# Optimization experiments

Measured on AMD Instinct MI355X. Metric: run time of the kernel, lower is better.

## Reference

```python
import jax, jax.numpy as jnp
import numpy as np

NUM_USERS = 100000
NUM_ITEMS = 50000
N = NUM_USERS + NUM_ITEMS
EMB = 64
NNZ = 4000000
B = 4096
GAMMA = 1.0
REG_LAMBDA = 1e-4
T_END = 1.0  # Euler step size: t = [0, 1]
EPS = 1e-12


def setup_inputs() -> dict:
    key = jax.random.key(0)
    ks = jax.random.split(key, 8)
    user = jax.random.randint(ks[0], (B,), 0, NUM_USERS)
    positive = jax.random.randint(ks[1], (B,), 0, NUM_ITEMS)
    negative = jax.random.randint(ks[2], (B,), 0, NUM_ITEMS)
    adj_rows = jax.random.randint(ks[3], (NNZ,), 0, N)
    adj_cols = jax.random.randint(ks[4], (NNZ,), 0, N)
    # normalized-adjacency-like small positive values
    adj_vals = jax.random.uniform(ks[5], (NNZ,), jnp.float32) * 1e-3
    user_emb = jax.random.normal(ks[6], (NUM_USERS, EMB), jnp.float32) * 0.1
    item_emb = jax.random.normal(ks[7], (NUM_ITEMS, EMB), jnp.float32) * 0.1
    return {
        "user": user, "positive": positive, "negative": negative,
        "adj_rows": adj_rows, "adj_cols": adj_cols, "adj_vals": adj_vals,
        "user_emb": user_emb, "item_emb": item_emb,
    }


def _normalize(x):
    return x * jax.lax.rsqrt(jnp.sum(x * x, axis=-1, keepdims=True) + EPS)


def _uniform_loss(x):
    # log mean_{i<j} exp(-2 * ||xn_i - xn_j||^2), xn = L2-normalized
    xn = _normalize(x)
    sq = jnp.maximum(2.0 - 2.0 * (xn @ xn.T), 0.0)  # [B, B] pairwise squared dist
    mask = jnp.triu(jnp.ones((x.shape[0], x.shape[0]), bool), k=1)
    vals = jnp.where(mask, jnp.exp(-2.0 * sq), 0.0)
    n_pairs = x.shape[0] * (x.shape[0] - 1) / 2.0
    return jnp.log(jnp.sum(vals) / n_pairs)


def reference(user, positive, negative, adj_rows, adj_cols, adj_vals, user_emb, item_emb):
    # ego embeddings: concat user/item tables -> [N, EMB]
    x = jnp.concatenate([user_emb, item_emb], axis=0)
    # sparse spmm: ax = A @ x (COO gather + segment reduce)
    ax = jax.ops.segment_sum(adj_vals[:, None] * x[adj_cols], adj_rows, num_segments=N)
    # ODEFunc f(t, x) = A@x + e with e = x0; one Euler step z1 = x0 + t*(A@x0 + x0)
    z = x + T_END * (ax + x)
    u_all, i_all = z[:NUM_USERS], z[NUM_USERS:]
    u = u_all[user]          # [B, EMB]
    i = i_all[positive]      # [B, EMB]
    # alignment loss on normalized embeddings
    un, inn = _normalize(u), _normalize(i)
    align = jnp.mean(jnp.sum((un - inn) ** 2, axis=-1))
    # uniformity loss
    uniform = GAMMA * (_uniform_loss(u) + _uniform_loss(i)) / 2.0
    # L2 reg on ego (pre-propagation) embeddings
    ego_u = user_emb[user]
    ego_i = item_emb[positive]
    reg = REG_LAMBDA * 0.5 * (jnp.sum(ego_u ** 2) + jnp.sum(ego_i ** 2)) / B
    return jnp.stack([align, uniform, reg])
```

## Files before the change

kernel.cpp:

```cpp
#include <hip/hip_runtime.h>
#include <math.h>

#define NUSERS 100000
#define NITEMS 50000
#define NN (NUSERS + NITEMS)
#define EMB 64
#define NNZ_ 4000000
#define BB 4096
#define NSLOT (2 * BB)
#define CAP 128
#define BMW 4688
#define EPSN 1e-12f
#define NT 32
#define NTRI 528


typedef __attribute__((ext_vector_type(8))) short short8v;
typedef __attribute__((ext_vector_type(16))) float f32x16;

__device__ inline float wave_reduce_sum(float v) {
  #pragma unroll
  for (int off = 32; off >= 1; off >>= 1) v += __shfl_xor(v, off, 64);
  return v;
}

__device__ inline unsigned short f2bf(float f) {
  unsigned u = __float_as_uint(f);
  unsigned r = u + 0x7fffu + ((u >> 16) & 1u);
  return (unsigned short)(r >> 16);
}

__global__ __launch_bounds__(256) void lg_init(int* map, int* fillp, unsigned* bitmap) {
  int t = blockIdx.x * blockDim.x + threadIdx.x;
  if (t < NN) map[t] = -1;
  if (t < NSLOT) fillp[t] = 0;
  if (t < BMW) bitmap[t] = 0u;
}

__global__ __launch_bounds__(256) void lg_mark(const int* __restrict__ user,
                                               const int* __restrict__ positive,
                                               int* __restrict__ map,
                                               unsigned* __restrict__ bitmap) {
  int t = blockIdx.x * blockDim.x + threadIdx.x;
  if (t >= 2 * BB) return;
  int row = (t < BB) ? user[t] : (NUSERS + positive[t - BB]);
  atomicCAS(&map[row], -1, t);
  atomicOr(&bitmap[row >> 5], 1u << (row & 31));
}

__device__ inline void lg_bin_one(int r, int c, float v, const unsigned* bm,
                                  const int* map, int* fillp, uint2* bins) {
  if ((bm[r >> 5] >> (r & 31)) & 1u) {
    int s = map[r];
    int pos = atomicAdd(&fillp[s], 1);
    if (pos < CAP) {
      uint2 e; e.x = (unsigned)c; e.y = __float_as_uint(v);
      bins[(size_t)s * CAP + pos] = e;
    }
  }
}

__global__ __launch_bounds__(256) void lg_scan_bin(const int4* __restrict__ rows4,
                                                   const int4* __restrict__ cols4,
                                                   const float4* __restrict__ vals4,
                                                   const unsigned* __restrict__ bitmap,
                                                   const int* __restrict__ map,
                                                   int* __restrict__ fillp,
                                                   uint2* __restrict__ bins) {
  __shared__ unsigned bm[BMW];
  for (int i = threadIdx.x; i < BMW; i += 256) bm[i] = bitmap[i];
  __syncthreads();
  const int STRIDE = 2048 * 256;
  const int NG = NNZ_ / 4;
  int g0 = blockIdx.x * 256 + threadIdx.x;
  int g1 = g0 + STRIDE;
  int4 r0 = rows4[g0];
  int4 c0 = cols4[g0];
  float4 v0 = vals4[g0];
  bool has1 = (g1 < NG);
  int4 r1 = {}, c1 = {};
  float4 v1 = {};
  if (has1) {
    r1 = rows4[g1];
    c1 = cols4[g1];
    v1 = vals4[g1];
  }
  lg_bin_one(r0.x, c0.x, v0.x, bm, map, fillp, bins);
  lg_bin_one(r0.y, c0.y, v0.y, bm, map, fillp, bins);
  lg_bin_one(r0.z, c0.z, v0.z, bm, map, fillp, bins);
  lg_bin_one(r0.w, c0.w, v0.w, bm, map, fillp, bins);
  if (has1) {
    lg_bin_one(r1.x, c1.x, v1.x, bm, map, fillp, bins);
    lg_bin_one(r1.y, c1.y, v1.y, bm, map, fillp, bins);
    lg_bin_one(r1.z, c1.z, v1.z, bm, map, fillp, bins);
    lg_bin_one(r1.w, c1.w, v1.w, bm, map, fillp, bins);
  }
}

__global__ __launch_bounds__(256) void lg_accum(const int* __restrict__ fillp,
                                                const uint2* __restrict__ bins,
                                                const float* __restrict__ uemb,
                                                const float* __restrict__ iemb,
                                                float* __restrict__ acc) {
  int w = (blockIdx.x * blockDim.x + threadIdx.x) >> 6;
  int lane = threadIdx.x & 63;
  if (w >= NSLOT) return;
  int n = min(fillp[w], CAP);
  const uint2* bs = bins + (size_t)w * CAP;
  float a = 0.0f;
  int k = 0;
  for (; k + 4 <= n; k += 4) {
    uint2 e0 = bs[k];
    uint2 e1 = bs[k + 1];
    uint2 e2 = bs[k + 2];
    uint2 e3 = bs[k + 3];
    int c0 = (int)e0.x; float v0 = __uint_as_float(e0.y);
    int c1 = (int)e1.x; float v1 = __uint_as_float(e1.y);
    int c2 = (int)e2.x; float v2 = __uint_as_float(e2.y);
    int c3 = (int)e3.x; float v3 = __uint_as_float(e3.y);
    const float* x0 = (c0 < NUSERS) ? uemb + (size_t)c0 * EMB : iemb + (size_t)(c0 - NUSERS) * EMB;
    const float* x1 = (c1 < NUSERS) ? uemb + (size_t)c1 * EMB : iemb + (size_t)(c1 - NUSERS) * EMB;
    const float* x2 = (c2 < NUSERS) ? uemb + (size_t)c2 * EMB : iemb + (size_t)(c2 - NUSERS) * EMB;
    const float* x3 = (c3 < NUSERS) ? uemb + (size_t)c3 * EMB : iemb + (size_t)(c3 - NUSERS) * EMB;
    float f0 = x0[lane], f1 = x1[lane], f2 = x2[lane], f3 = x3[lane];
    a = fmaf(v0, f0, a);
    a = fmaf(v1, f1, a);
    a = fmaf(v2, f2, a);
    a = fmaf(v3, f3, a);
  }
  for (; k < n; ++k) {
    uint2 e0 = bs[k];
    int c0 = (int)e0.x; float v0 = __uint_as_float(e0.y);
    const float* x0 = (c0 < NUSERS) ? uemb + (size_t)c0 * EMB : iemb + (size_t)(c0 - NUSERS) * EMB;
    a = fmaf(v0, x0[lane], a);
  }
  acc[(size_t)w * EMB + lane] = a;
}

__global__ __launch_bounds__(256) void lg_prep(const int* __restrict__ user,
                                               const int* __restrict__ positive,
                                               const float* __restrict__ uemb,
                                               const float* __restrict__ iemb,
                                               const int* __restrict__ map,
                                               const float* __restrict__ acc,
                                               unsigned short* __restrict__ zub,
                                               unsigned short* __restrict__ zib,
                                               float* __restrict__ part_align,
                                               float* __restrict__ part_reg) {
  int w = (blockIdx.x * blockDim.x + threadIdx.x) >> 6;
  int lane = threadIdx.x & 63;
  if (w >= BB) return;
  int ru = user[w];
  int pi = positive[w];
  float eu = uemb[(size_t)ru * EMB + lane];
  float ei = iemb[(size_t)pi * EMB + lane];
  int su = map[ru];
  int si = map[NUSERS + pi];
  float zul = 2.0f * eu + acc[(size_t)su * EMB + lane];
  float zil = 2.0f * ei + acc[(size_t)si * EMB + lane];
  float nu = wave_reduce_sum(zul * zul);
  float ni = wave_reduce_sum(zil * zil);
  float un = zul * rsqrtf(nu + EPSN);
  float inn = zil * rsqrtf(ni + EPSN);
  zub[(size_t)w * EMB + lane] = f2bf(un);
  zib[(size_t)w * EMB + lane] = f2bf(inn);
  float d = un - inn;
  float align_b = wave_reduce_sum(d * d);
  float reg_b = wave_reduce_sum(eu * eu + ei * ei);
  if (lane == 0) {
    part_align[w] = align_b;
    part_reg[w] = reg_b;
  }
}

__global__ __launch_bounds__(256) void lg_gram_mfma(const unsigned short* __restrict__ zub,
                                                    const unsigned short* __restrict__ zib,
                                                    float* __restrict__ gpart) {
  int L = blockIdx.x, m = blockIdx.y;
  int ib = 0, rem = L;
  while (rem >= NT - ib) { rem -= NT - ib; ++ib; }
  int jb = ib + rem;
  const unsigned short* z = (m == 0) ? zub : zib;
  __shared__ float wsum[4];
  int t = threadIdx.x;
  int l = t & 63, w = t >> 6;
  int wr = w >> 1, wc = w & 1;
  int lr = l & 31;
  int koff = (l >> 5) * 8;
  const short8v* pa0 = (const short8v*)(z + (size_t)(ib * 128 + wr * 64 + lr) * EMB + koff);
  const short8v* pa1 = (const short8v*)(z + (size_t)(ib * 128 + wr * 64 + 32 + lr) * EMB + koff);
  const short8v* pb0 = (const short8v*)(z + (size_t)(jb * 128 + wc * 64 + lr) * EMB + koff);
  const short8v* pb1 = (const short8v*)(z + (size_t)(jb * 128 + wc * 64 + 32 + lr) * EMB + koff);
  f32x16 a00 = {}, a01 = {}, a10 = {}, a11 = {};
  #pragma unroll
  for (int ks = 0; ks < 4; ++ks) {
    short8v a0 = pa0[ks * 2];
    short8v a1 = pa1[ks * 2];
    short8v b0 = pb0[ks * 2];
    short8v b1 = pb1[ks * 2];
    a00 = __builtin_amdgcn_mfma_f32_32x32x16_bf16(a0, b0, a00, 0, 0, 0);
    a01 = __builtin_amdgcn_mfma_f32_32x32x16_bf16(a0, b1, a01, 0, 0, 0);
    a10 = __builtin_amdgcn_mfma_f32_32x32x16_bf16(a1, b0, a10, 0, 0, 0);
    a11 = __builtin_amdgcn_mfma_f32_32x32x16_bf16(a1, b1, a11, 0, 0, 0);
  }
  float s = 0.0f;
  #pragma unroll
  for (int e = 0; e < 16; ++e) {
    s += __expf(-2.0f * fmaxf(fmaf(-2.0f, a00[e], 2.0f), 0.0f));
    s += __expf(-2.0f * fmaxf(fmaf(-2.0f, a01[e], 2.0f), 0.0f));
    s += __expf(-2.0f * fmaxf(fmaf(-2.0f, a10[e], 2.0f), 0.0f));
    s += __expf(-2.0f * fmaxf(fmaf(-2.0f, a11[e], 2.0f), 0.0f));
  }
  s = wave_reduce_sum(s);
  if (l == 0) wsum[w] = s;
  __syncthreads();
  if (t == 0) {
    float tot = wsum[0] + wsum[1] + wsum[2] + wsum[3];
    float wgt = (ib == jb) ? 1.0f : 2.0f;
    gpart[m * NTRI + L] = wgt * tot;
  }
}

__global__ __launch_bounds__(256) void lg_final(const float* __restrict__ part_align,
                                                const float* __restrict__ part_reg,
                                                const float* __restrict__ gpart,
                                                float* __restrict__ out) {
  __shared__ float red[4][4];
  int t = threadIdx.x;
  float sa = 0.0f, sr = 0.0f, su = 0.0f, si = 0.0f;
  for (int k = t; k < 4096; k += 256) {
    sa += part_align[k];
    sr += part_reg[k];
  }
  for (int k = t; k < NTRI; k += 256) {
    su += gpart[k];
    si += gpart[NTRI + k];
  }
  sa = wave_reduce_sum(sa);
  sr = wave_reduce_sum(sr);
  su = wave_reduce_sum(su);
  si = wave_reduce_sum(si);
  if ((t & 63) == 0) {
    int wid = t >> 6;
    red[wid][0] = sa; red[wid][1] = sr; red[wid][2] = su; red[wid][3] = si;
  }
  __syncthreads();
  if (t == 0) {
    float a = 0, r = 0, Su = 0, Si = 0;
    #pragma unroll
    for (int wv = 0; wv < 4; ++wv) {
      a += red[wv][0]; r += red[wv][1]; Su += red[wv][2]; Si += red[wv][3];
    }
    float align = a / (float)BB;
    float reg = 1e-4f * 0.5f * r / (float)BB;
    float npairs = (float)BB * (float)(BB - 1) * 0.5f;
    float tri_u = (Su - (float)BB) * 0.5f;
    float tri_i = (Si - (float)BB) * 0.5f;
    float Lu = logf(tri_u / npairs);
    float Li = logf(tri_i / npairs);
    out[0] = align;
    out[1] = 0.5f * (Lu + Li);
    out[2] = reg;
  }
}

extern "C" void kernel_launch(void* const* d_in, const int* in_sizes, int n_in,
                              void* d_out, int out_size, void* d_ws, size_t ws_size,
                              hipStream_t stream) {
  const int* user = (const int*)d_in[0];
  const int* positive = (const int*)d_in[1];
  const int* adj_rows = (const int*)d_in[3];
  const int* adj_cols = (const int*)d_in[4];
  const float* adj_vals = (const float*)d_in[5];
  const float* uemb = (const float*)d_in[6];
  const float* iemb = (const float*)d_in[7];

  char* ws = (char*)d_ws;
  int* map = (int*)(ws);
  int* fillp = (int*)(ws + (1u << 20));
  uint2* bins = (uint2*)(ws + (2u << 20));
  float* acc = (float*)(ws + (10u << 20));
  unsigned short* zub = (unsigned short*)(ws + (12u << 20));
  unsigned short* zib = (unsigned short*)(ws + (12u << 20) + (512u << 10));
  float* part_align = (float*)(ws + (13u << 20));
  float* part_reg = (float*)(ws + (13u << 20) + (16u << 10));
  float* gpart = (float*)(ws + (13u << 20) + (32u << 10));
  unsigned* bitmap = (unsigned*)(ws + (13u << 20) + (64u << 10));
  float* out = (float*)d_out;

  lg_init<<<dim3(1024), dim3(256), 0, stream>>>(map, fillp, bitmap);
  lg_mark<<<dim3(32), dim3(256), 0, stream>>>(user, positive, map, bitmap);
  lg_scan_bin<<<dim3(2048), dim3(256), 0, stream>>>(
      (const int4*)adj_rows, (const int4*)adj_cols, (const float4*)adj_vals,
      bitmap, map, fillp, bins);
  lg_accum<<<dim3(NSLOT / 4), dim3(256), 0, stream>>>(fillp, bins, uemb, iemb, acc);
  lg_prep<<<dim3(1024), dim3(256), 0, stream>>>(user, positive, uemb, iemb, map,
                                                acc, zub, zib, part_align, part_reg);
  lg_gram_mfma<<<dim3(NTRI, 2), dim3(256), 0, stream>>>(zub, zib, gpart);
  lg_final<<<dim3(1), dim3(256), 0, stream>>>(part_align, part_reg, gpart, out);
}
```

Baseline: 67.29 us.

## Compact matching edges per wave with ballot before binning atomics

The scan kernel no longer stages the whole row bitmap in shared memory per block. It reads the bitmap directly from global/L2, one int4 group per thread. Matching edges are compacted into a per-wave shared queue using ballot/popcount, and the queue is drained by consecutive lanes so the map lookups and atomics run with dense lane use instead of divergent per-element branches. The grid grows to cover all groups with one per thread, which adds more blocks but removes the per-block 18KB bitmap copy and sync.

```diff
diff --git a/kernel.cpp b/kernel.cpp
--- a/kernel.cpp
+++ b/kernel.cpp
@@ -48,18 +48,6 @@
   atomicOr(&bitmap[row >> 5], 1u << (row & 31));
 }
 
-__device__ inline void lg_bin_one(int r, int c, float v, const unsigned* bm,
-                                  const int* map, int* fillp, uint2* bins) {
-  if ((bm[r >> 5] >> (r & 31)) & 1u) {
-    int s = map[r];
-    int pos = atomicAdd(&fillp[s], 1);
-    if (pos < CAP) {
-      uint2 e; e.x = (unsigned)c; e.y = __float_as_uint(v);
-      bins[(size_t)s * CAP + pos] = e;
-    }
-  }
-}
-
 __global__ __launch_bounds__(256) void lg_scan_bin(const int4* __restrict__ rows4,
                                                    const int4* __restrict__ cols4,
                                                    const float4* __restrict__ vals4,
@@ -67,33 +55,53 @@
                                                    const int* __restrict__ map,
                                                    int* __restrict__ fillp,
                                                    uint2* __restrict__ bins) {
-  __shared__ unsigned bm[BMW];
-  for (int i = threadIdx.x; i < BMW; i += 256) bm[i] = bitmap[i];
-  __syncthreads();
-  const int STRIDE = 2048 * 256;
+  __shared__ int qr[4][256];
+  __shared__ uint2 qcv[4][256];
+  int t = threadIdx.x;
+  int lane = t & 63, w = t >> 6;
+  unsigned long long lmlt = (1ull << lane) - 1ull;
   const int NG = NNZ_ / 4;
-  int g0 = blockIdx.x * 256 + threadIdx.x;
-  int g1 = g0 + STRIDE;
-  int4 r0 = rows4[g0];
-  int4 c0 = cols4[g0];
-  float4 v0 = vals4[g0];
-  bool has1 = (g1 < NG);
-  int4 r1 = {}, c1 = {};
-  float4 v1 = {};
-  if (has1) {
-    r1 = rows4[g1];
-    c1 = cols4[g1];
-    v1 = vals4[g1];
-  }
-  lg_bin_one(r0.x, c0.x, v0.x, bm, map, fillp, bins);
-  lg_bin_one(r0.y, c0.y, v0.y, bm, map, fillp, bins);
-  lg_bin_one(r0.z, c0.z, v0.z, bm, map, fillp, bins);
-  lg_bin_one(r0.w, c0.w, v0.w, bm, map, fillp, bins);
-  if (has1) {
-    lg_bin_one(r1.x, c1.x, v1.x, bm, map, fillp, bins);
-    lg_bin_one(r1.y, c1.y, v1.y, bm, map, fillp, bins);
-    lg_bin_one(r1.z, c1.z, v1.z, bm, map, fillp, bins);
-    lg_bin_one(r1.w, c1.w, v1.w, bm, map, fillp, bins);
+  int g = blockIdx.x * 256 + t;
+  bool valid = g < NG;
+  int gg = valid ? g : 0;
+  int4 r = rows4[gg];
+  int4 c = cols4[gg];
+  float4 v = vals4[gg];
+  bool h0 = valid && ((bitmap[r.x >> 5] >> (r.x & 31)) & 1u);
+  bool h1 = valid && ((bitmap[r.y >> 5] >> (r.y & 31)) & 1u);
+  bool h2 = valid && ((bitmap[r.z >> 5] >> (r.z & 31)) & 1u);
+  bool h3 = valid && ((bitmap[r.w >> 5] >> (r.w & 31)) & 1u);
+  int qn = 0;
+  {
+    unsigned long long m = __ballot(h0);
+    if (h0) { int p = qn + (int)__popcll(m & lmlt); qr[w][p] = r.x;
+              qcv[w][p] = make_uint2((unsigned)c.x, __float_as_uint(v.x)); }
+    qn += (int)__popcll(m);
+  }
+  {
+    unsigned long long m = __ballot(h1);
+    if (h1) { int p = qn + (int)__popcll(m & lmlt); qr[w][p] = r.y;
+              qcv[w][p] = make_uint2((unsigned)c.y, __float_as_uint(v.y)); }
+    qn += (int)__popcll(m);
+  }
+  {
+    unsigned long long m = __ballot(h2);
+    if (h2) { int p = qn + (int)__popcll(m & lmlt); qr[w][p] = r.z;
+              qcv[w][p] = make_uint2((unsigned)c.z, __float_as_uint(v.z)); }
+    qn += (int)__popcll(m);
+  }
+  {
+    unsigned long long m = __ballot(h3);
+    if (h3) { int p = qn + (int)__popcll(m & lmlt); qr[w][p] = r.w;
+              qcv[w][p] = make_uint2((unsigned)c.w, __float_as_uint(v.w)); }
+    qn += (int)__popcll(m);
+  }
+  for (int i = lane; i < qn; i += 64) {
+    int rr = qr[w][i];
+    uint2 cv = qcv[w][i];
+    int s = map[rr];
+    int pos = atomicAdd(&fillp[s], 1);
+    if (pos < CAP) bins[(size_t)s * CAP + pos] = cv;
   }
 }
 
@@ -288,9 +296,10 @@
   unsigned* bitmap = (unsigned*)(ws + (13u << 20) + (64u << 10));
   float* out = (float*)d_out;
 
+  const int NG = NNZ_ / 4;
   lg_init<<<dim3(1024), dim3(256), 0, stream>>>(map, fillp, bitmap);
   lg_mark<<<dim3(32), dim3(256), 0, stream>>>(user, positive, map, bitmap);
-  lg_scan_bin<<<dim3(2048), dim3(256), 0, stream>>>(
+  lg_scan_bin<<<dim3((NG + 255) / 256), dim3(256), 0, stream>>>(
       (const int4*)adj_rows, (const int4*)adj_cols, (const float4*)adj_vals,
       bitmap, map, fillp, bins);
   lg_accum<<<dim3(NSLOT / 4), dim3(256), 0, stream>>>(fillp, bins, uemb, iemb, acc);
```

Measured after the change: 66.72 us. Within noise of the previous version (-0.8%).
